# Kernel tuning notes

Measured on AMD Instinct MI355X. Metric: run time of the kernel, lower is better.

## Reference

```python
import jax, jax.numpy as jnp
import numpy as np

F8_MAX = 448.0  # max representable value of float8_e4m3fn


def setup_inputs() -> dict:
    key = jax.random.key(0)
    k1, k2, k3 = jax.random.split(key, 3)
    inp = jax.random.normal(k1, (4, 2048, 4096), dtype=jnp.float32)
    weight = jax.random.normal(k2, (4096, 16384), dtype=jnp.float32) * 0.02  # [in, out] (stored transposed)
    bias = jax.random.normal(k3, (16384,), dtype=jnp.float32)
    return {"inp": inp, "weight": weight, "bias": bias}


def reference(inp, weight, bias):
    # --- weight quantization (from_float with abs-max observer) ---
    w_scale = jnp.max(jnp.abs(weight)) / F8_MAX                      # scalar fp32
    w_q = (weight * (1.0 / w_scale)).astype(jnp.float8_e4m3fn)       # [in, out] fp8

    # --- dynamic input quantization: amax = max(|min|, |max|) ---
    x = inp.reshape(-1, inp.shape[-1])                               # [N, in]
    amax = jnp.maximum(jnp.abs(jnp.min(x)), jnp.abs(jnp.max(x)))
    x_scale = amax / F8_MAX
    x_q = (x * (1.0 / x_scale)).astype(jnp.float8_e4m3fn)            # [N, in] fp8

    # --- fp8_gemm_v2: dequant-matmul with fused scales + bias ---
    out = jnp.matmul(x_q.astype(jnp.float32), w_q.astype(jnp.float32))
    out = out * (x_scale * w_scale) + bias                           # [N, out]
    return out.reshape(inp.shape[:-1] + (weight.shape[1],))
```

## Files before the change

kernel.cpp:

```cpp
#include <hip/hip_runtime.h>
#include <stdint.h>
#include <stddef.h>

typedef float f32x16 __attribute__((ext_vector_type(16)));
typedef int i32x8 __attribute__((ext_vector_type(8)));

union Frag32 { long l[4]; i32x8 v; };


__device__ __forceinline__ float max4(const float4 v) {
  return fmaxf(fmaxf(fabsf(v.x), fabsf(v.y)), fmaxf(fabsf(v.z), fabsf(v.w)));
}

__global__ void absmax_both_kernel(const float4* __restrict__ w, size_t wn4,
                                   const float4* __restrict__ x, size_t xn4,
                                   unsigned int* __restrict__ out) {
  const size_t tid0 = (size_t)blockIdx.x * blockDim.x + threadIdx.x;
  const size_t stride = (size_t)gridDim.x * blockDim.x * 4;
  float mw = 0.f, mx = 0.f;
  for (size_t i = tid0 * 4; i < wn4; i += stride) {
    float a = max4(w[i]), b = max4(w[i + 1]);
    float c = max4(w[i + 2]), d = max4(w[i + 3]);
    mw = fmaxf(mw, fmaxf(fmaxf(a, b), fmaxf(c, d)));
  }
  for (size_t i = tid0 * 4; i < xn4; i += stride) {
    float a = max4(x[i]), b = max4(x[i + 1]);
    float c = max4(x[i + 2]), d = max4(x[i + 3]);
    mx = fmaxf(mx, fmaxf(fmaxf(a, b), fmaxf(c, d)));
  }
#pragma unroll
  for (int off = 32; off > 0; off >>= 1) {
    mw = fmaxf(mw, __shfl_xor(mw, off));
    mx = fmaxf(mx, __shfl_xor(mx, off));
  }
  if ((threadIdx.x & 63) == 0) {
    atomicMax(out + 0, __float_as_uint(mw));
    atomicMax(out + 1, __float_as_uint(mx));
  }
}

__global__ void quantize_x_kernel(const float4* __restrict__ x,
                                  uint8_t* __restrict__ xq,
                                  const unsigned int* __restrict__ amax,
                                  int K, int ksh, int n_chunks) {
  const float x_scale = __uint_as_float(amax[1]) / 448.0f;
  const float inv = 1.0f / x_scale;
  int idx = blockIdx.x * blockDim.x + threadIdx.x;
  const int stride = gridDim.x * blockDim.x;
  for (; idx < n_chunks; idx += stride) {
    const int slot = idx >> 9;
    const int p16 = idx & 511;
    const int row = p16 >> 1;
    const int kkb0 = (p16 & 1) << 4;
    const int mblk = slot >> ksh;
    const int ksl = slot & ((1 << ksh) - 1);
    const size_t f4 = ((size_t)(mblk * 256 + row) * K + ksl * 32 + kkb0) >> 2;
    const float4 v0 = x[f4 + 0], v1 = x[f4 + 1], v2 = x[f4 + 2], v3 = x[f4 + 3];
    uint32_t c0 = __builtin_amdgcn_cvt_pk_fp8_f32(v0.x * inv, v0.y * inv, 0, false);
    c0 = __builtin_amdgcn_cvt_pk_fp8_f32(v0.z * inv, v0.w * inv, c0, true);
    uint32_t c1 = __builtin_amdgcn_cvt_pk_fp8_f32(v1.x * inv, v1.y * inv, 0, false);
    c1 = __builtin_amdgcn_cvt_pk_fp8_f32(v1.z * inv, v1.w * inv, c1, true);
    uint32_t c2 = __builtin_amdgcn_cvt_pk_fp8_f32(v2.x * inv, v2.y * inv, 0, false);
    c2 = __builtin_amdgcn_cvt_pk_fp8_f32(v2.z * inv, v2.w * inv, c2, true);
    uint32_t c3 = __builtin_amdgcn_cvt_pk_fp8_f32(v3.x * inv, v3.y * inv, 0, false);
    c3 = __builtin_amdgcn_cvt_pk_fp8_f32(v3.z * inv, v3.w * inv, c3, true);
    const unsigned long long L0 = (unsigned long long)c0 | ((unsigned long long)c1 << 32);
    const unsigned long long L1 = (unsigned long long)c2 | ((unsigned long long)c3 << 32);
    const int Lc = row * 32 + kkb0;
    const int mask = ((row >> 2) & 3) << 3;
    const int addr0 = Lc ^ (mask & 16);
    uint8_t* p = xq + (size_t)slot * 8192;
    *(unsigned long long*)(p + addr0 + (mask & 8)) = L0;
    *(unsigned long long*)(p + addr0 + (8 ^ (mask & 8))) = L1;
  }
}

__global__ void quantize_wT_kernel(const float* __restrict__ w,
                                   uint8_t* __restrict__ wqt,
                                   const unsigned int* __restrict__ amax,
                                   int N, int K) {
  __shared__ float tileF[64][129];
  const float w_scale = __uint_as_float(amax[0]) / 448.0f;
  const float inv = 1.0f / w_scale;
  const int tn = blockIdx.x;
  const int tk = blockIdx.y;
  const int t = threadIdx.x;
  {
    const int nn4 = t & 15;
    const int kk0 = t >> 4;
#pragma unroll
    for (int i = 0; i < 8; ++i) {
      const int kk = kk0 + i * 16;
      const float4 v =
          *(const float4*)&w[(size_t)(tk * 128 + kk) * N + tn * 64 + nn4 * 4];
      tileF[nn4 * 4 + 0][kk] = v.x;
      tileF[nn4 * 4 + 1][kk] = v.y;
      tileF[nn4 * 4 + 2][kk] = v.z;
      tileF[nn4 * 4 + 3][kk] = v.w;
    }
  }
  __syncthreads();
  {
    const int n = t & 63;
    const int c = t >> 6;
    unsigned long long q[4];
#pragma unroll
    for (int cc = 0; cc < 4; ++cc) {
      const float4 u0 = *(const float4*)&tileF[n][c * 32 + cc * 8];
      const float4 u1 = *(const float4*)&tileF[n][c * 32 + cc * 8 + 4];
      uint32_t lo = __builtin_amdgcn_cvt_pk_fp8_f32(u0.x * inv, u0.y * inv, 0, false);
      lo = __builtin_amdgcn_cvt_pk_fp8_f32(u0.z * inv, u0.w * inv, lo, true);
      uint32_t hi = __builtin_amdgcn_cvt_pk_fp8_f32(u1.x * inv, u1.y * inv, 0, false);
      hi = __builtin_amdgcn_cvt_pk_fp8_f32(u1.z * inv, u1.w * inv, hi, true);
      q[cc] = (unsigned long long)lo | ((unsigned long long)hi << 32);
    }
    const int n_g = tn * 64 + n;
    const int k0g = tk * 128 + c * 32;
    const size_t slot = (size_t)(n_g >> 8) * (K >> 5) + (k0g >> 5);
    const int row = n_g & 255;
    const int m2 = (row >> 2) & 3;
    ulonglong2 s0, s1;
    s0.x = q[0 ^ m2]; s0.y = q[1 ^ m2];
    s1.x = q[2 ^ m2]; s1.y = q[3 ^ m2];
    uint8_t* pbase = wqt + slot * 8192 + row * 32;
    *(ulonglong2*)(pbase) = s0;
    *(ulonglong2*)(pbase + 16) = s1;
  }
}

#define T_BM 256
#define T_BN 256
#define UNIT_SCALE 0x7F7F7F7F

__device__ __forceinline__ void gl_lds16(const uint8_t* g, uint8_t* lds) {
  __builtin_amdgcn_global_load_lds(
      (const __attribute__((address_space(1))) void*)g,
      (__attribute__((address_space(3))) void*)lds, 16, 0, 0);
}

__global__ __launch_bounds__(1024, 4) void gemm_fp8_mx(
    const uint8_t* __restrict__ Aq, const uint8_t* __restrict__ BqT,
    const float* __restrict__ bias, const unsigned int* __restrict__ amax,
    float* __restrict__ C, int M, int N, int K) {
  extern __shared__ uint8_t smem[];
  uint8_t* const Ar = smem;
  uint8_t* const Br = smem + 65536;

  const int ntm = M / T_BM;
  const int mpx = ntm >> 3;
  const int bid = blockIdx.x;
  const int s = bid >> 3;
  const int tm = (bid & 7) * mpx + (s & (mpx - 1));
  const int tn = s / mpx;
  const int m0 = tm * T_BM;
  const int n0 = tn * T_BN;

  const int tid = threadIdx.x;
  const int w = tid >> 6;
  const int l = tid & 63;
  const int wr = w >> 2;
  const int wc = w & 3;

  const int kslots = K >> 5;

  const int soff = w * 1024 + l * 16;
  const uint8_t* a_src = Aq + (size_t)(m0 >> 8) * kslots * 8192 + soff;
  const uint8_t* b_src = BqT + (size_t)(n0 >> 8) * kslots * 8192 + soff;

  const int h = l >> 5;
  const int rl = l & 31;
  int aoff[2][4], boff[2][4];
#pragma unroll
  for (int mt = 0; mt < 2; ++mt) {
    const int ra = wr * 64 + mt * 32 + rl;
    const int rb = wc * 64 + mt * 32 + rl;
#pragma unroll
    for (int j = 0; j < 4; ++j) {
      aoff[mt][j] = h * 8192 + ra * 32 + ((j ^ ((ra >> 2) & 3)) * 8);
      boff[mt][j] = h * 8192 + rb * 32 + ((j ^ ((rb >> 2) & 3)) * 8);
    }
  }

  f32x16 acc[2][2];
#pragma unroll
  for (int i = 0; i < 2; ++i)
#pragma unroll
    for (int j = 0; j < 2; ++j) acc[i][j] = 0.f;

  const int NP = K >> 6;

  gl_lds16(a_src, Ar + soff);
  gl_lds16(b_src, Br + soff);
  gl_lds16(a_src + 16384, Ar + 16384 + soff);
  gl_lds16(b_src + 16384, Br + 16384 + soff);
  asm volatile("s_waitcnt vmcnt(2)" ::: "memory");
  __builtin_amdgcn_s_barrier();

  for (int p = 0; p < NP; ++p) {
    const int ss = (p + 2 < NP) ? (p + 2) : (p - 2);
    const int rslot = ((p + 2) & 3) * 16384;
    gl_lds16(a_src + (size_t)ss * 16384, Ar + rslot + soff);
    gl_lds16(b_src + (size_t)ss * 16384, Br + rslot + soff);

    const uint8_t* Asl = Ar + (p & 3) * 16384;
    const uint8_t* Bsl = Br + (p & 3) * 16384;
    Frag32 af[2], bf[2];
#pragma unroll
    for (int t2 = 0; t2 < 2; ++t2)
#pragma unroll
      for (int j = 0; j < 4; ++j) {
        af[t2].l[j] = *(const long*)(Asl + aoff[t2][j]);
        bf[t2].l[j] = *(const long*)(Bsl + boff[t2][j]);
      }

    __builtin_amdgcn_s_setprio(1);
    acc[0][0] = __builtin_amdgcn_mfma_scale_f32_32x32x64_f8f6f4(
        af[0].v, bf[0].v, acc[0][0], 0, 0, 0, UNIT_SCALE, 0, UNIT_SCALE);
    acc[1][0] = __builtin_amdgcn_mfma_scale_f32_32x32x64_f8f6f4(
        af[1].v, bf[0].v, acc[1][0], 0, 0, 0, UNIT_SCALE, 0, UNIT_SCALE);
    acc[0][1] = __builtin_amdgcn_mfma_scale_f32_32x32x64_f8f6f4(
        af[0].v, bf[1].v, acc[0][1], 0, 0, 0, UNIT_SCALE, 0, UNIT_SCALE);
    acc[1][1] = __builtin_amdgcn_mfma_scale_f32_32x32x64_f8f6f4(
        af[1].v, bf[1].v, acc[1][1], 0, 0, 0, UNIT_SCALE, 0, UNIT_SCALE);
    __builtin_amdgcn_s_setprio(0);

    asm volatile("s_waitcnt vmcnt(2)" ::: "memory");
    __builtin_amdgcn_s_barrier();
  }
  asm volatile("s_waitcnt vmcnt(0)" ::: "memory");

  const float x_scale = __uint_as_float(amax[1]) / 448.0f;
  const float w_scale = __uint_as_float(amax[0]) / 448.0f;
  const float sc = x_scale * w_scale;
  const int colb = n0 + wc * 64 + rl;
  const int rowb = m0 + wr * 64 + 4 * h;
#pragma unroll
  for (int nt = 0; nt < 2; ++nt) {
    const int col = colb + nt * 32;
    const float bv = bias[col];
#pragma unroll
    for (int mt = 0; mt < 2; ++mt) {
#pragma unroll
      for (int r = 0; r < 16; ++r) {
        const int row = rowb + mt * 32 + (r & 3) + 8 * (r >> 2);
        C[(size_t)row * N + col] = acc[mt][nt][r] * sc + bv;
      }
    }
  }
}

extern "C" void kernel_launch(void* const* d_in, const int* in_sizes, int n_in,
                              void* d_out, int out_size, void* d_ws, size_t ws_size,
                              hipStream_t stream) {
  const float* inp = (const float*)d_in[0];
  const float* weight = (const float*)d_in[1];
  const float* bias = (const float*)d_in[2];
  float* out = (float*)d_out;

  const int N = in_sizes[2];
  const int K = in_sizes[1] / N;
  const int M = in_sizes[0] / K;

  uint8_t* ws = (uint8_t*)d_ws;
  unsigned int* amax = (unsigned int*)ws;
  uint8_t* xq = ws + 256;
  uint8_t* wqt = ws + 256 + (size_t)M * K;

  int ksh = 0;
  while ((1 << (ksh + 5)) < K) ++ksh;

  hipMemsetAsync(d_ws, 0, 8, stream);

  absmax_both_kernel<<<2048, 256, 0, stream>>>(
      (const float4*)weight, (size_t)K * N / 4,
      (const float4*)inp, (size_t)M * K / 4, amax);

  quantize_x_kernel<<<4096, 256, 0, stream>>>((const float4*)inp, xq, amax,
                                              K, ksh, M * K / 16);
  quantize_wT_kernel<<<dim3(N / 64, K / 128), 256, 0, stream>>>(weight, wqt,
                                                                amax, N, K);

  gemm_fp8_mx<<<(M / T_BM) * (N / T_BN), 1024, 131072, stream>>>(
      xq, wqt, bias, amax, out, M, N, K);
}
```

Baseline: 861.2 us.

## Load A fragments directly from global memory into registers, staging only B in LDS

The x quantizer now writes each 16-byte chunk unswizzled, so every lane's A fragment is contiguous. The GEMM then reads A straight from global memory into registers instead of staging it through LDS, and only B goes through the LDS ring buffer. This halves shared memory per block and removes the LDS reads for A. In exchange every wave issues its own global loads of A each k-step, with less latency hiding and duplicate reads across the waves that share rows. The wait counts are restructured around the new loads.

```diff
diff --git a/kernel.cpp b/kernel.cpp
--- a/kernel.cpp
+++ b/kernel.cpp
@@ -64,14 +64,9 @@
     c2 = __builtin_amdgcn_cvt_pk_fp8_f32(v2.z * inv, v2.w * inv, c2, true);
     uint32_t c3 = __builtin_amdgcn_cvt_pk_fp8_f32(v3.x * inv, v3.y * inv, 0, false);
     c3 = __builtin_amdgcn_cvt_pk_fp8_f32(v3.z * inv, v3.w * inv, c3, true);
-    const unsigned long long L0 = (unsigned long long)c0 | ((unsigned long long)c1 << 32);
-    const unsigned long long L1 = (unsigned long long)c2 | ((unsigned long long)c3 << 32);
-    const int Lc = row * 32 + kkb0;
-    const int mask = ((row >> 2) & 3) << 3;
-    const int addr0 = Lc ^ (mask & 16);
-    uint8_t* p = xq + (size_t)slot * 8192;
-    *(unsigned long long*)(p + addr0 + (mask & 8)) = L0;
-    *(unsigned long long*)(p + addr0 + (8 ^ (mask & 8))) = L1;
+    uint4 o;
+    o.x = c0; o.y = c1; o.z = c2; o.w = c3;
+    *(uint4*)(xq + (size_t)slot * 8192 + row * 32 + kkb0) = o;
   }
 }
 
@@ -143,8 +138,7 @@
     const float* __restrict__ bias, const unsigned int* __restrict__ amax,
     float* __restrict__ C, int M, int N, int K) {
   extern __shared__ uint8_t smem[];
-  uint8_t* const Ar = smem;
-  uint8_t* const Br = smem + 65536;
+  uint8_t* const Br = smem;
 
   const int ntm = M / T_BM;
   const int mpx = ntm >> 3;
@@ -164,21 +158,20 @@
   const int kslots = K >> 5;
 
   const int soff = w * 1024 + l * 16;
-  const uint8_t* a_src = Aq + (size_t)(m0 >> 8) * kslots * 8192 + soff;
   const uint8_t* b_src = BqT + (size_t)(n0 >> 8) * kslots * 8192 + soff;
 
   const int h = l >> 5;
   const int rl = l & 31;
-  int aoff[2][4], boff[2][4];
+  const uint8_t* a_ptr = Aq + (size_t)(m0 >> 8) * kslots * 8192 +
+                         h * 8192 + (wr * 64 + rl) * 32;
+
+  int boff[2][4];
 #pragma unroll
   for (int mt = 0; mt < 2; ++mt) {
-    const int ra = wr * 64 + mt * 32 + rl;
     const int rb = wc * 64 + mt * 32 + rl;
 #pragma unroll
-    for (int j = 0; j < 4; ++j) {
-      aoff[mt][j] = h * 8192 + ra * 32 + ((j ^ ((ra >> 2) & 3)) * 8);
+    for (int j = 0; j < 4; ++j)
       boff[mt][j] = h * 8192 + rb * 32 + ((j ^ ((rb >> 2) & 3)) * 8);
-    }
   }
 
   f32x16 acc[2][2];
@@ -189,29 +182,34 @@
 
   const int NP = K >> 6;
 
-  gl_lds16(a_src, Ar + soff);
   gl_lds16(b_src, Br + soff);
-  gl_lds16(a_src + 16384, Ar + 16384 + soff);
   gl_lds16(b_src + 16384, Br + 16384 + soff);
-  asm volatile("s_waitcnt vmcnt(2)" ::: "memory");
+  asm volatile("s_waitcnt vmcnt(1)" ::: "memory");
   __builtin_amdgcn_s_barrier();
 
   for (int p = 0; p < NP; ++p) {
-    const int ss = (p + 2 < NP) ? (p + 2) : (p - 2);
-    const int rslot = ((p + 2) & 3) * 16384;
-    gl_lds16(a_src + (size_t)ss * 16384, Ar + rslot + soff);
-    gl_lds16(b_src + (size_t)ss * 16384, Br + rslot + soff);
-
-    const uint8_t* Asl = Ar + (p & 3) * 16384;
+    const uint8_t* ap = a_ptr + (size_t)p * 16384;
+    Frag32 af[2];
+#pragma unroll
+    for (int mt = 0; mt < 2; ++mt) {
+      ulonglong2 t0 = *(const ulonglong2*)(ap + mt * 1024);
+      ulonglong2 t1 = *(const ulonglong2*)(ap + mt * 1024 + 16);
+      af[mt].l[0] = (long)t0.x; af[mt].l[1] = (long)t0.y;
+      af[mt].l[2] = (long)t1.x; af[mt].l[3] = (long)t1.y;
+    }
+
+    const int ss = (p + 2 < NP) ? (p + 2) : (NP - 1);
+    gl_lds16(b_src + (size_t)ss * 16384, Br + ((p + 2) & 3) * 16384 + soff);
+
     const uint8_t* Bsl = Br + (p & 3) * 16384;
-    Frag32 af[2], bf[2];
-#pragma unroll
-    for (int t2 = 0; t2 < 2; ++t2)
-#pragma unroll
-      for (int j = 0; j < 4; ++j) {
-        af[t2].l[j] = *(const long*)(Asl + aoff[t2][j]);
-        bf[t2].l[j] = *(const long*)(Bsl + boff[t2][j]);
-      }
+    Frag32 bf[2];
+#pragma unroll
+    for (int mt = 0; mt < 2; ++mt)
+#pragma unroll
+      for (int j = 0; j < 4; ++j)
+        bf[mt].l[j] = *(const long*)(Bsl + boff[mt][j]);
+
+    asm volatile("s_waitcnt vmcnt(1)" ::: "memory");
 
     __builtin_amdgcn_s_setprio(1);
     acc[0][0] = __builtin_amdgcn_mfma_scale_f32_32x32x64_f8f6f4(
@@ -224,7 +222,6 @@
         af[1].v, bf[1].v, acc[1][1], 0, 0, 0, UNIT_SCALE, 0, UNIT_SCALE);
     __builtin_amdgcn_s_setprio(0);
 
-    asm volatile("s_waitcnt vmcnt(2)" ::: "memory");
     __builtin_amdgcn_s_barrier();
   }
   asm volatile("s_waitcnt vmcnt(0)" ::: "memory");
@@ -280,6 +277,6 @@
   quantize_wT_kernel<<<dim3(N / 64, K / 128), 256, 0, stream>>>(weight, wqt,
                                                                 amax, N, K);
 
-  gemm_fp8_mx<<<(M / T_BM) * (N / T_BN), 1024, 131072, stream>>>(
+  gemm_fp8_mx<<<(M / T_BM) * (N / T_BN), 1024, 65536, stream>>>(
       xq, wqt, bias, amax, out, M, N, K);
 }
```

Result: slower. 1.075 ms (+24.8%).

## Fuse absmax and both quantization kernels into one cooperative prep kernel

Applied to the files above, without the earlier changes.

Merges the absmax reduction, input quantization and weight transpose-quantization into a single cooperative kernel that does a grid-wide sync after the atomic max reduction. This removes two kernel launches and the launch gaps between them. In exchange the grid is capped at 1024 blocks of 256 threads, and the weight tiles are processed in a grid-stride loop, so parallelism and latency hiding may drop compared with the original 2D grid of thousands of blocks. The grid sync also adds a barrier cost.

```diff
diff --git a/kernel.cpp b/kernel.cpp
--- a/kernel.cpp
+++ b/kernel.cpp
@@ -1,4 +1,5 @@
 #include <hip/hip_runtime.h>
+#include <hip/hip_cooperative_groups.h>
 #include <stdint.h>
 #include <stddef.h>
 
@@ -12,119 +13,123 @@
   return fmaxf(fmaxf(fabsf(v.x), fabsf(v.y)), fmaxf(fabsf(v.z), fabsf(v.w)));
 }
 
-__global__ void absmax_both_kernel(const float4* __restrict__ w, size_t wn4,
-                                   const float4* __restrict__ x, size_t xn4,
-                                   unsigned int* __restrict__ out) {
-  const size_t tid0 = (size_t)blockIdx.x * blockDim.x + threadIdx.x;
-  const size_t stride = (size_t)gridDim.x * blockDim.x * 4;
-  float mw = 0.f, mx = 0.f;
-  for (size_t i = tid0 * 4; i < wn4; i += stride) {
-    float a = max4(w[i]), b = max4(w[i + 1]);
-    float c = max4(w[i + 2]), d = max4(w[i + 3]);
-    mw = fmaxf(mw, fmaxf(fmaxf(a, b), fmaxf(c, d)));
-  }
-  for (size_t i = tid0 * 4; i < xn4; i += stride) {
-    float a = max4(x[i]), b = max4(x[i + 1]);
-    float c = max4(x[i + 2]), d = max4(x[i + 3]);
-    mx = fmaxf(mx, fmaxf(fmaxf(a, b), fmaxf(c, d)));
-  }
-#pragma unroll
-  for (int off = 32; off > 0; off >>= 1) {
-    mw = fmaxf(mw, __shfl_xor(mw, off));
-    mx = fmaxf(mx, __shfl_xor(mx, off));
-  }
-  if ((threadIdx.x & 63) == 0) {
-    atomicMax(out + 0, __float_as_uint(mw));
-    atomicMax(out + 1, __float_as_uint(mx));
-  }
-}
-
-__global__ void quantize_x_kernel(const float4* __restrict__ x,
-                                  uint8_t* __restrict__ xq,
-                                  const unsigned int* __restrict__ amax,
-                                  int K, int ksh, int n_chunks) {
+__global__ void prep_kernel(const float4* __restrict__ w, size_t wn4,
+                            const float4* __restrict__ x, size_t xn4,
+                            uint8_t* __restrict__ wqt, uint8_t* __restrict__ xq,
+                            unsigned int* __restrict__ amax,
+                            int N, int K, int ksh, int xchunks, int wtiles) {
+  __shared__ float tileF[64][129];
+  const int t = threadIdx.x;
+
+  {
+    const size_t tid0 = (size_t)blockIdx.x * blockDim.x + t;
+    const size_t stride = (size_t)gridDim.x * blockDim.x * 4;
+    float mw = 0.f, mx = 0.f;
+    for (size_t i = tid0 * 4; i < wn4; i += stride) {
+      float a = max4(w[i]), b = max4(w[i + 1]);
+      float c = max4(w[i + 2]), d = max4(w[i + 3]);
+      mw = fmaxf(mw, fmaxf(fmaxf(a, b), fmaxf(c, d)));
+    }
+    for (size_t i = tid0 * 4; i < xn4; i += stride) {
+      float a = max4(x[i]), b = max4(x[i + 1]);
+      float c = max4(x[i + 2]), d = max4(x[i + 3]);
+      mx = fmaxf(mx, fmaxf(fmaxf(a, b), fmaxf(c, d)));
+    }
+#pragma unroll
+    for (int off = 32; off > 0; off >>= 1) {
+      mw = fmaxf(mw, __shfl_xor(mw, off));
+      mx = fmaxf(mx, __shfl_xor(mx, off));
+    }
+    if ((t & 63) == 0) {
+      atomicMax(amax + 0, __float_as_uint(mw));
+      atomicMax(amax + 1, __float_as_uint(mx));
+    }
+  }
+  __threadfence();
+  cooperative_groups::this_grid().sync();
+
+  const float w_scale = __uint_as_float(amax[0]) / 448.0f;
   const float x_scale = __uint_as_float(amax[1]) / 448.0f;
-  const float inv = 1.0f / x_scale;
-  int idx = blockIdx.x * blockDim.x + threadIdx.x;
-  const int stride = gridDim.x * blockDim.x;
-  for (; idx < n_chunks; idx += stride) {
-    const int slot = idx >> 9;
-    const int p16 = idx & 511;
-    const int row = p16 >> 1;
-    const int kkb0 = (p16 & 1) << 4;
-    const int mblk = slot >> ksh;
-    const int ksl = slot & ((1 << ksh) - 1);
-    const size_t f4 = ((size_t)(mblk * 256 + row) * K + ksl * 32 + kkb0) >> 2;
-    const float4 v0 = x[f4 + 0], v1 = x[f4 + 1], v2 = x[f4 + 2], v3 = x[f4 + 3];
-    uint32_t c0 = __builtin_amdgcn_cvt_pk_fp8_f32(v0.x * inv, v0.y * inv, 0, false);
-    c0 = __builtin_amdgcn_cvt_pk_fp8_f32(v0.z * inv, v0.w * inv, c0, true);
-    uint32_t c1 = __builtin_amdgcn_cvt_pk_fp8_f32(v1.x * inv, v1.y * inv, 0, false);
-    c1 = __builtin_amdgcn_cvt_pk_fp8_f32(v1.z * inv, v1.w * inv, c1, true);
-    uint32_t c2 = __builtin_amdgcn_cvt_pk_fp8_f32(v2.x * inv, v2.y * inv, 0, false);
-    c2 = __builtin_amdgcn_cvt_pk_fp8_f32(v2.z * inv, v2.w * inv, c2, true);
-    uint32_t c3 = __builtin_amdgcn_cvt_pk_fp8_f32(v3.x * inv, v3.y * inv, 0, false);
-    c3 = __builtin_amdgcn_cvt_pk_fp8_f32(v3.z * inv, v3.w * inv, c3, true);
-    const unsigned long long L0 = (unsigned long long)c0 | ((unsigned long long)c1 << 32);
-    const unsigned long long L1 = (unsigned long long)c2 | ((unsigned long long)c3 << 32);
-    const int Lc = row * 32 + kkb0;
-    const int mask = ((row >> 2) & 3) << 3;
-    const int addr0 = Lc ^ (mask & 16);
-    uint8_t* p = xq + (size_t)slot * 8192;
-    *(unsigned long long*)(p + addr0 + (mask & 8)) = L0;
-    *(unsigned long long*)(p + addr0 + (8 ^ (mask & 8))) = L1;
-  }
-}
-
-__global__ void quantize_wT_kernel(const float* __restrict__ w,
-                                   uint8_t* __restrict__ wqt,
-                                   const unsigned int* __restrict__ amax,
-                                   int N, int K) {
-  __shared__ float tileF[64][129];
-  const float w_scale = __uint_as_float(amax[0]) / 448.0f;
-  const float inv = 1.0f / w_scale;
-  const int tn = blockIdx.x;
-  const int tk = blockIdx.y;
-  const int t = threadIdx.x;
+  const float winv = 1.0f / w_scale;
+  const float xinv = 1.0f / x_scale;
+
   {
-    const int nn4 = t & 15;
-    const int kk0 = t >> 4;
-#pragma unroll
-    for (int i = 0; i < 8; ++i) {
-      const int kk = kk0 + i * 16;
-      const float4 v =
-          *(const float4*)&w[(size_t)(tk * 128 + kk) * N + tn * 64 + nn4 * 4];
-      tileF[nn4 * 4 + 0][kk] = v.x;
-      tileF[nn4 * 4 + 1][kk] = v.y;
-      tileF[nn4 * 4 + 2][kk] = v.z;
-      tileF[nn4 * 4 + 3][kk] = v.w;
-    }
-  }
-  __syncthreads();
-  {
-    const int n = t & 63;
-    const int c = t >> 6;
-    unsigned long long q[4];
-#pragma unroll
-    for (int cc = 0; cc < 4; ++cc) {
-      const float4 u0 = *(const float4*)&tileF[n][c * 32 + cc * 8];
-      const float4 u1 = *(const float4*)&tileF[n][c * 32 + cc * 8 + 4];
-      uint32_t lo = __builtin_amdgcn_cvt_pk_fp8_f32(u0.x * inv, u0.y * inv, 0, false);
-      lo = __builtin_amdgcn_cvt_pk_fp8_f32(u0.z * inv, u0.w * inv, lo, true);
-      uint32_t hi = __builtin_amdgcn_cvt_pk_fp8_f32(u1.x * inv, u1.y * inv, 0, false);
-      hi = __builtin_amdgcn_cvt_pk_fp8_f32(u1.z * inv, u1.w * inv, hi, true);
-      q[cc] = (unsigned long long)lo | ((unsigned long long)hi << 32);
-    }
-    const int n_g = tn * 64 + n;
-    const int k0g = tk * 128 + c * 32;
-    const size_t slot = (size_t)(n_g >> 8) * (K >> 5) + (k0g >> 5);
-    const int row = n_g & 255;
-    const int m2 = (row >> 2) & 3;
-    ulonglong2 s0, s1;
-    s0.x = q[0 ^ m2]; s0.y = q[1 ^ m2];
-    s1.x = q[2 ^ m2]; s1.y = q[3 ^ m2];
-    uint8_t* pbase = wqt + slot * 8192 + row * 32;
-    *(ulonglong2*)(pbase) = s0;
-    *(ulonglong2*)(pbase + 16) = s1;
+    int idx = blockIdx.x * blockDim.x + t;
+    const int stride = gridDim.x * blockDim.x;
+    for (; idx < xchunks; idx += stride) {
+      const int slot = idx >> 9;
+      const int p16 = idx & 511;
+      const int row = p16 >> 1;
+      const int kkb0 = (p16 & 1) << 4;
+      const int mblk = slot >> ksh;
+      const int ksl = slot & ((1 << ksh) - 1);
+      const size_t f4 = ((size_t)(mblk * 256 + row) * K + ksl * 32 + kkb0) >> 2;
+      const float4 v0 = x[f4 + 0], v1 = x[f4 + 1], v2 = x[f4 + 2], v3 = x[f4 + 3];
+      uint32_t c0 = __builtin_amdgcn_cvt_pk_fp8_f32(v0.x * xinv, v0.y * xinv, 0, false);
+      c0 = __builtin_amdgcn_cvt_pk_fp8_f32(v0.z * xinv, v0.w * xinv, c0, true);
+      uint32_t c1 = __builtin_amdgcn_cvt_pk_fp8_f32(v1.x * xinv, v1.y * xinv, 0, false);
+      c1 = __builtin_amdgcn_cvt_pk_fp8_f32(v1.z * xinv, v1.w * xinv, c1, true);
+      uint32_t c2 = __builtin_amdgcn_cvt_pk_fp8_f32(v2.x * xinv, v2.y * xinv, 0, false);
+      c2 = __builtin_amdgcn_cvt_pk_fp8_f32(v2.z * xinv, v2.w * xinv, c2, true);
+      uint32_t c3 = __builtin_amdgcn_cvt_pk_fp8_f32(v3.x * xinv, v3.y * xinv, 0, false);
+      c3 = __builtin_amdgcn_cvt_pk_fp8_f32(v3.z * xinv, v3.w * xinv, c3, true);
+      const unsigned long long L0 = (unsigned long long)c0 | ((unsigned long long)c1 << 32);
+      const unsigned long long L1 = (unsigned long long)c2 | ((unsigned long long)c3 << 32);
+      const int Lc = row * 32 + kkb0;
+      const int mask = ((row >> 2) & 3) << 3;
+      const int addr0 = Lc ^ (mask & 16);
+      uint8_t* p = xq + (size_t)slot * 8192;
+      *(unsigned long long*)(p + addr0 + (mask & 8)) = L0;
+      *(unsigned long long*)(p + addr0 + (8 ^ (mask & 8))) = L1;
+    }
+  }
+
+  const int ntn = N >> 6;
+  for (int tile = blockIdx.x; tile < wtiles; tile += gridDim.x) {
+    const int tn = tile % ntn;
+    const int tk = tile / ntn;
+    __syncthreads();
+    {
+      const int nn4 = t & 15;
+      const int kk0 = t >> 4;
+#pragma unroll
+      for (int i = 0; i < 8; ++i) {
+        const int kk = kk0 + i * 16;
+        const float4 v =
+            *(const float4*)&w[((size_t)(tk * 128 + kk) * N + tn * 64 + nn4 * 4) >> 2];
+        tileF[nn4 * 4 + 0][kk] = v.x;
+        tileF[nn4 * 4 + 1][kk] = v.y;
+        tileF[nn4 * 4 + 2][kk] = v.z;
+        tileF[nn4 * 4 + 3][kk] = v.w;
+      }
+    }
+    __syncthreads();
+    {
+      const int n = t & 63;
+      const int c = t >> 6;
+      unsigned long long q[4];
+#pragma unroll
+      for (int cc = 0; cc < 4; ++cc) {
+        const float4 u0 = *(const float4*)&tileF[n][c * 32 + cc * 8];
+        const float4 u1 = *(const float4*)&tileF[n][c * 32 + cc * 8 + 4];
+        uint32_t lo = __builtin_amdgcn_cvt_pk_fp8_f32(u0.x * winv, u0.y * winv, 0, false);
+        lo = __builtin_amdgcn_cvt_pk_fp8_f32(u0.z * winv, u0.w * winv, lo, true);
+        uint32_t hi = __builtin_amdgcn_cvt_pk_fp8_f32(u1.x * winv, u1.y * winv, 0, false);
+        hi = __builtin_amdgcn_cvt_pk_fp8_f32(u1.z * winv, u1.w * winv, hi, true);
+        q[cc] = (unsigned long long)lo | ((unsigned long long)hi << 32);
+      }
+      const int n_g = tn * 64 + n;
+      const int k0g = tk * 128 + c * 32;
+      const size_t slot = (size_t)(n_g >> 8) * (K >> 5) + (k0g >> 5);
+      const int row = n_g & 255;
+      const int m2 = (row >> 2) & 3;
+      ulonglong2 s0, s1;
+      s0.x = q[0 ^ m2]; s0.y = q[1 ^ m2];
+      s1.x = q[2 ^ m2]; s1.y = q[3 ^ m2];
+      uint8_t* pbase = wqt + slot * 8192 + row * 32;
+      *(ulonglong2*)(pbase) = s0;
+      *(ulonglong2*)(pbase + 16) = s1;
+    }
   }
 }
 
@@ -271,14 +276,16 @@
 
   hipMemsetAsync(d_ws, 0, 8, stream);
 
-  absmax_both_kernel<<<2048, 256, 0, stream>>>(
-      (const float4*)weight, (size_t)K * N / 4,
-      (const float4*)inp, (size_t)M * K / 4, amax);
-
-  quantize_x_kernel<<<4096, 256, 0, stream>>>((const float4*)inp, xq, amax,
-                                              K, ksh, M * K / 16);
-  quantize_wT_kernel<<<dim3(N / 64, K / 128), 256, 0, stream>>>(weight, wqt,
-                                                                amax, N, K);
+  const float4* w4 = (const float4*)weight;
+  const float4* x4 = (const float4*)inp;
+  size_t wn4 = (size_t)K * N / 4;
+  size_t xn4 = (size_t)M * K / 4;
+  int xchunks = M * K / 16;
+  int wtiles = (N / 64) * (K / 128);
+  void* args[] = {&w4, &wn4, &x4, &xn4, &wqt, &xq, &amax,
+                  (void*)&N, (void*)&K, &ksh, &xchunks, &wtiles};
+  hipLaunchCooperativeKernel((const void*)prep_kernel, dim3(1024), dim3(256),
+                             args, 0, stream);
 
   gemm_fp8_mx<<<(M / T_BM) * (N / T_BN), 1024, 131072, stream>>>(
       xq, wqt, bias, amax, out, M, N, K);
```

Measured after the change: 972.4 us. +12.9%, slower.

## Pre-pack FP8 operands in MFMA fragment order for 16-byte LDS reads

Applied to the files above, without the earlier changes.

The quantization kernels now write X and W^T in a layout where each lane's 16-byte MFMA fragment pieces sit contiguously, in 16 KB k-slices grouped by 32-row blocks. The GEMM loads each fragment with two 16-byte LDS reads instead of four 8-byte reads and no longer needs the XOR swizzle. The X quantizer also reads input rows sequentially along K, so global reads coalesce better. The cost is new store patterns in the quantizers and possible LDS bank behaviour changes in the GEMM.

```diff
diff --git a/kernel.cpp b/kernel.cpp
--- a/kernel.cpp
+++ b/kernel.cpp
@@ -42,19 +42,20 @@
 __global__ void quantize_x_kernel(const float4* __restrict__ x,
                                   uint8_t* __restrict__ xq,
                                   const unsigned int* __restrict__ amax,
-                                  int K, int ksh, int n_chunks) {
+                                  int K, int ks16, int n_chunks) {
   const float x_scale = __uint_as_float(amax[1]) / 448.0f;
   const float inv = 1.0f / x_scale;
   int idx = blockIdx.x * blockDim.x + threadIdx.x;
   const int stride = gridDim.x * blockDim.x;
   for (; idx < n_chunks; idx += stride) {
-    const int slot = idx >> 9;
-    const int p16 = idx & 511;
-    const int row = p16 >> 1;
-    const int kkb0 = (p16 & 1) << 4;
-    const int mblk = slot >> ksh;
-    const int ksl = slot & ((1 << ksh) - 1);
-    const size_t f4 = ((size_t)(mblk * 256 + row) * K + ksl * 32 + kkb0) >> 2;
+    const int row_g = idx >> ks16;
+    const int kc16 = idx & ((1 << ks16) - 1);
+    const int mblk = row_g >> 8;
+    const int row = row_g & 255;
+    const int s = kc16 >> 2;
+    const int kh = (kc16 >> 1) & 1;
+    const int c = kc16 & 1;
+    const size_t f4 = (size_t)row_g * (K >> 2) + kc16 * 4;
     const float4 v0 = x[f4 + 0], v1 = x[f4 + 1], v2 = x[f4 + 2], v3 = x[f4 + 3];
     uint32_t c0 = __builtin_amdgcn_cvt_pk_fp8_f32(v0.x * inv, v0.y * inv, 0, false);
     c0 = __builtin_amdgcn_cvt_pk_fp8_f32(v0.z * inv, v0.w * inv, c0, true);
@@ -64,14 +65,11 @@
     c2 = __builtin_amdgcn_cvt_pk_fp8_f32(v2.z * inv, v2.w * inv, c2, true);
     uint32_t c3 = __builtin_amdgcn_cvt_pk_fp8_f32(v3.x * inv, v3.y * inv, 0, false);
     c3 = __builtin_amdgcn_cvt_pk_fp8_f32(v3.z * inv, v3.w * inv, c3, true);
-    const unsigned long long L0 = (unsigned long long)c0 | ((unsigned long long)c1 << 32);
-    const unsigned long long L1 = (unsigned long long)c2 | ((unsigned long long)c3 << 32);
-    const int Lc = row * 32 + kkb0;
-    const int mask = ((row >> 2) & 3) << 3;
-    const int addr0 = Lc ^ (mask & 16);
-    uint8_t* p = xq + (size_t)slot * 8192;
-    *(unsigned long long*)(p + addr0 + (mask & 8)) = L0;
-    *(unsigned long long*)(p + addr0 + (8 ^ (mask & 8))) = L1;
+    uint4 o;
+    o.x = c0; o.y = c1; o.z = c2; o.w = c3;
+    uint8_t* dst = xq + ((size_t)(mblk * (K >> 6) + s)) * 16384 +
+                   (row >> 5) * 2048 + c * 1024 + kh * 512 + (row & 31) * 16;
+    *(uint4*)dst = o;
   }
 }
 
@@ -102,12 +100,12 @@
   __syncthreads();
   {
     const int n = t & 63;
-    const int c = t >> 6;
+    const int ck = t >> 6;
     unsigned long long q[4];
 #pragma unroll
     for (int cc = 0; cc < 4; ++cc) {
-      const float4 u0 = *(const float4*)&tileF[n][c * 32 + cc * 8];
-      const float4 u1 = *(const float4*)&tileF[n][c * 32 + cc * 8 + 4];
+      const float4 u0 = *(const float4*)&tileF[n][ck * 32 + cc * 8];
+      const float4 u1 = *(const float4*)&tileF[n][ck * 32 + cc * 8 + 4];
       uint32_t lo = __builtin_amdgcn_cvt_pk_fp8_f32(u0.x * inv, u0.y * inv, 0, false);
       lo = __builtin_amdgcn_cvt_pk_fp8_f32(u0.z * inv, u0.w * inv, lo, true);
       uint32_t hi = __builtin_amdgcn_cvt_pk_fp8_f32(u1.x * inv, u1.y * inv, 0, false);
@@ -115,16 +113,17 @@
       q[cc] = (unsigned long long)lo | ((unsigned long long)hi << 32);
     }
     const int n_g = tn * 64 + n;
-    const int k0g = tk * 128 + c * 32;
-    const size_t slot = (size_t)(n_g >> 8) * (K >> 5) + (k0g >> 5);
+    const int k0g = tk * 128 + ck * 32;
+    const int s = k0g >> 6;
+    const int kh = (k0g >> 5) & 1;
     const int row = n_g & 255;
-    const int m2 = (row >> 2) & 3;
+    uint8_t* base = wqt + ((size_t)((n_g >> 8) * (K >> 6) + s)) * 16384 +
+                    (row >> 5) * 2048 + kh * 512 + (row & 31) * 16;
     ulonglong2 s0, s1;
-    s0.x = q[0 ^ m2]; s0.y = q[1 ^ m2];
-    s1.x = q[2 ^ m2]; s1.y = q[3 ^ m2];
-    uint8_t* pbase = wqt + slot * 8192 + row * 32;
-    *(ulonglong2*)(pbase) = s0;
-    *(ulonglong2*)(pbase + 16) = s1;
+    s0.x = q[0]; s0.y = q[1];
+    s1.x = q[2]; s1.y = q[3];
+    *(ulonglong2*)(base) = s0;
+    *(ulonglong2*)(base + 1024) = s1;
   }
 }
 
@@ -161,23 +160,21 @@
   const int wr = w >> 2;
   const int wc = w & 3;
 
-  const int kslots = K >> 5;
+  const int kslices = K >> 6;
 
   const int soff = w * 1024 + l * 16;
-  const uint8_t* a_src = Aq + (size_t)(m0 >> 8) * kslots * 8192 + soff;
-  const uint8_t* b_src = BqT + (size_t)(n0 >> 8) * kslots * 8192 + soff;
+  const uint8_t* a_src = Aq + (size_t)(m0 >> 8) * kslices * 16384 + soff;
+  const uint8_t* b_src = BqT + (size_t)(n0 >> 8) * kslices * 16384 + soff;
 
   const int h = l >> 5;
   const int rl = l & 31;
-  int aoff[2][4], boff[2][4];
+  int aoff[2][2], boff[2][2];
 #pragma unroll
   for (int mt = 0; mt < 2; ++mt) {
-    const int ra = wr * 64 + mt * 32 + rl;
-    const int rb = wc * 64 + mt * 32 + rl;
-#pragma unroll
-    for (int j = 0; j < 4; ++j) {
-      aoff[mt][j] = h * 8192 + ra * 32 + ((j ^ ((ra >> 2) & 3)) * 8);
-      boff[mt][j] = h * 8192 + rb * 32 + ((j ^ ((rb >> 2) & 3)) * 8);
+#pragma unroll
+    for (int c = 0; c < 2; ++c) {
+      aoff[mt][c] = (wr * 2 + mt) * 2048 + c * 1024 + l * 16;
+      boff[mt][c] = (wc * 2 + mt) * 2048 + c * 1024 + l * 16;
     }
   }
 
@@ -206,12 +203,16 @@
     const uint8_t* Bsl = Br + (p & 3) * 16384;
     Frag32 af[2], bf[2];
 #pragma unroll
-    for (int t2 = 0; t2 < 2; ++t2)
-#pragma unroll
-      for (int j = 0; j < 4; ++j) {
-        af[t2].l[j] = *(const long*)(Asl + aoff[t2][j]);
-        bf[t2].l[j] = *(const long*)(Bsl + boff[t2][j]);
-      }
+    for (int mt = 0; mt < 2; ++mt) {
+      ulonglong2 a0 = *(const ulonglong2*)(Asl + aoff[mt][0]);
+      ulonglong2 a1 = *(const ulonglong2*)(Asl + aoff[mt][1]);
+      af[mt].l[0] = (long)a0.x; af[mt].l[1] = (long)a0.y;
+      af[mt].l[2] = (long)a1.x; af[mt].l[3] = (long)a1.y;
+      ulonglong2 b0 = *(const ulonglong2*)(Bsl + boff[mt][0]);
+      ulonglong2 b1 = *(const ulonglong2*)(Bsl + boff[mt][1]);
+      bf[mt].l[0] = (long)b0.x; bf[mt].l[1] = (long)b0.y;
+      bf[mt].l[2] = (long)b1.x; bf[mt].l[3] = (long)b1.y;
+    }
 
     __builtin_amdgcn_s_setprio(1);
     acc[0][0] = __builtin_amdgcn_mfma_scale_f32_32x32x64_f8f6f4(
@@ -266,8 +267,8 @@
   uint8_t* xq = ws + 256;
   uint8_t* wqt = ws + 256 + (size_t)M * K;
 
-  int ksh = 0;
-  while ((1 << (ksh + 5)) < K) ++ksh;
+  int ks16 = 0;
+  while ((1 << (ks16 + 4)) < K) ++ks16;
 
   hipMemsetAsync(d_ws, 0, 8, stream);
 
@@ -276,7 +277,7 @@
       (const float4*)inp, (size_t)M * K / 4, amax);
 
   quantize_x_kernel<<<4096, 256, 0, stream>>>((const float4*)inp, xq, amax,
-                                              K, ksh, M * K / 16);
+                                              K, ks16, M * K / 16);
   quantize_wT_kernel<<<dim3(N / 64, K / 128), 256, 0, stream>>>(weight, wqt,
                                                                 amax, N, K);
 
```

Result: slower. 993.8 us (+15.4%).
